# Kernel tuning notes

Measured on AMD Instinct MI355X. Metric: run time of the kernel, lower is better.

## Reference

```python
import jax, jax.numpy as jnp
import numpy as np

B, C_IN, H, W = 32, 3, 256, 256
PATCH = 16
E, C_OUT = 8, 8
C_PROJ = 16
NUM_CLASSES = 1000
SPP_LEVELS = (1, 2, 4)
GATE_STEEPNESS = 10.0


def _conv(x, w, b, pad):
    # x: [N,C,H,W], w: [O,C,kh,kw]
    y = jax.lax.conv_general_dilated(x, w, (1, 1), [(pad, pad), (pad, pad)],
                                     dimension_numbers=('NCHW', 'OIHW', 'NCHW'))
    return y + b[None, :, None, None]


def _forward(X, expert_w, expert_b, proj_w, proj_b, keys, threshold,
             final_w, final_b, lin_w, lin_b):
    Bx, C, Hx, Wx = X.shape
    h, w = Hx // PATCH, Wx // PATCH
    P = h * w
    # 1) patch extraction: [B,C,H,W] -> [B*P, C, ph, pw]
    xp = (X.reshape(Bx, C, h, PATCH, w, PATCH)
           .transpose(0, 2, 4, 1, 3, 5)
           .reshape(Bx * P, C, PATCH, PATCH))
    # 2) router: conv projection -> global avg pool -> key similarity -> softmax -> soft threshold gate
    proj = _conv(xp, proj_w, proj_b, 1)                 # [BP, 16, ph, pw]
    pooled = proj.mean(axis=(2, 3))                     # [BP, 16]
    scores = jax.nn.softmax(pooled @ keys.T, axis=-1)   # [BP, E]
    gate = scores * jax.nn.sigmoid((scores - threshold) * GATE_STEEPNESS)
    gate = gate / (gate.sum(axis=-1, keepdims=True) + 1e-9)
    gate = gate.reshape(Bx, P, E)
    # 3) all experts fused as one conv with E*C_OUT output channels (conv3x3 pad1 + ReLU)
    ew = expert_w.reshape(E * C_OUT, C, 3, 3)
    eb = expert_b.reshape(E * C_OUT)
    outs = jax.nn.relu(_conv(xp, ew, eb, 1))            # [BP, E*Cout, ph, pw]
    outs = outs.reshape(Bx, P, E, C_OUT, PATCH, PATCH)
    # 4) router-weighted combine over experts
    comb = jnp.einsum('bpe,bpeclm->bpclm', gate, outs)  # [B,P,Cout,ph,pw]
    # 5) reassemble patches -> [B, Cout, H, W]
    y = (comb.reshape(Bx, h, w, C_OUT, PATCH, PATCH)
             .transpose(0, 3, 1, 4, 2, 5)
             .reshape(Bx, C_OUT, h * PATCH, w * PATCH))
    # 6) final 1x1 conv with padding=4 (zero-pad input, bias added everywhere)
    ypad = jnp.pad(y, ((0, 0), (0, 0), (4, 4), (4, 4)))
    y = jnp.einsum('oc,bchw->bohw', final_w[:, :, 0, 0], ypad) + final_b[None, :, None, None]
    # 7) spatial pyramid pooling (levels 1,2,4) -> [B, Cout*21]
    Bc, Cc, Hc, Wc = y.shape
    feats = [y.reshape(Bc, Cc, l, Hc // l, l, Wc // l).mean(axis=(3, 5)).reshape(Bc, -1)
             for l in SPP_LEVELS]
    spp = jnp.concatenate(feats, axis=-1)
    # 8) classification head
    return spp @ lin_w + lin_b


def setup_inputs() -> dict:
    key = jax.random.key(0)
    ks = jax.random.split(key, 11)
    s = 0.1
    spp_dim = C_OUT * sum(l * l for l in SPP_LEVELS)  # 168
    return {
        'X': jax.random.normal(ks[0], (B, C_IN, H, W), jnp.float32),
        'expert_w': jax.random.normal(ks[1], (E, C_OUT, C_IN, 3, 3), jnp.float32) * s,
        'expert_b': jax.random.normal(ks[2], (E, C_OUT), jnp.float32) * s,
        'proj_w': jax.random.normal(ks[3], (C_PROJ, C_IN, 3, 3), jnp.float32) * s,
        'proj_b': jax.random.normal(ks[4], (C_PROJ,), jnp.float32) * s,
        'keys': jax.random.normal(ks[5], (E, C_PROJ), jnp.float32) * s,
        'threshold': jnp.array(0.125, jnp.float32),
        'final_w': jax.random.normal(ks[6], (C_OUT, C_OUT, 1, 1), jnp.float32) * s,
        'final_b': jax.random.normal(ks[7], (C_OUT,), jnp.float32) * s,
        'lin_w': jax.random.normal(ks[8], (spp_dim, NUM_CLASSES), jnp.float32) * s,
        'lin_b': jax.random.normal(ks[9], (NUM_CLASSES,), jnp.float32) * s,
    }


def reference(X, expert_w, expert_b, proj_w, proj_b, keys, threshold,
              final_w, final_b, lin_w, lin_b):
    return _forward(X, expert_w, expert_b, proj_w, proj_b, keys, threshold,
                    final_w, final_b, lin_w, lin_b)
```

## Files before the change

### kernel.cpp

```cpp
#include <hip/hip_runtime.h>
#include <hip/hip_bf16.h>
#include <math.h>


typedef short bf16x8 __attribute__((ext_vector_type(8)));
typedef float f32x4 __attribute__((ext_vector_type(4)));
typedef float pf2 __attribute__((ext_vector_type(2)));

__device__ __forceinline__ int cellOf(int r) {
    int rr = r + 4;
    return (rr >= 66) + (rr >= 132) + (rr >= 198);
}

__device__ __forceinline__ unsigned int packbf2(float lo, float hi) {
    __hip_bfloat162 h = __float22bfloat162_rn(make_float2(lo, hi));
    unsigned int u;
    __builtin_memcpy(&u, &h, 4);
    return u;
}

__global__ __launch_bounds__(256) void prep_kernel(
    const float* __restrict__ ew, const float* __restrict__ ebg,
    const float* __restrict__ pw, const float* __restrict__ pb,
    const float* __restrict__ keys, float* __restrict__ Sy,
    unsigned short* __restrict__ Bg, float* __restrict__ cbf)
{
    const int t = threadIdx.x;
    for (int i = t; i < 8192; i += 256) Sy[i] = 0.f;
    if (t < 72) {
        float sv[32];
        #pragma unroll
        for (int s = 0; s < 32; ++s) {
            int q, kx; bool zz = false;
            if (s < 16)       { q = s >> 1;  kx = s & 1; }
            else if (s < 18)  { q = 8;       kx = s - 16; }
            else if (s < 26)  { q = s - 18;  kx = 2; }
            else if (s == 26) { q = 8;       kx = 2; }
            else              { q = 0; kx = 0; zz = true; }
            const int ky = q / 3, c = q - ky * 3;
            const int widx = c * 9 + ky * 3 + kx;
            float a;
            if (t < 64) {
                a = ew[t * 27 + widx];
            } else {
                const int e = t - 64;
                a = 0.f;
                #pragma unroll
                for (int o = 0; o < 16; ++o)
                    a += keys[e * 16 + o] * pw[o * 27 + widx];
            }
            sv[s] = zz ? 0.f : a;
        }
        uint4 q0, q1, q2v, q3v;
        q0.x  = packbf2(sv[0],  sv[1]);  q0.y  = packbf2(sv[2],  sv[3]);
        q0.z  = packbf2(sv[4],  sv[5]);  q0.w  = packbf2(sv[6],  sv[7]);
        q1.x  = packbf2(sv[8],  sv[9]);  q1.y  = packbf2(sv[10], sv[11]);
        q1.z  = packbf2(sv[12], sv[13]); q1.w  = packbf2(sv[14], sv[15]);
        q2v.x = packbf2(sv[16], sv[17]); q2v.y = packbf2(sv[18], sv[19]);
        q2v.z = packbf2(sv[20], sv[21]); q2v.w = packbf2(sv[22], sv[23]);
        q3v.x = packbf2(sv[24], sv[25]); q3v.y = packbf2(sv[26], sv[27]);
        q3v.z = packbf2(sv[28], sv[29]); q3v.w = packbf2(sv[30], sv[31]);
        uint4* dst = reinterpret_cast<uint4*>(&Bg[t * 32]);
        dst[0] = q0; dst[1] = q1; dst[2] = q2v; dst[3] = q3v;
    }
    if (t >= 128 && t < 208) {
        const int i = t - 128;
        float c;
        if (i < 64) {
            c = ebg[i];
        } else {
            const int e = (i - 64) & 7;
            c = 0.f;
            #pragma unroll
            for (int o = 0; o < 16; ++o) c += keys[e * 16 + o] * pb[o];
        }
        cbf[i] = c;
    }
}

#define CONV_STEP(SB, ACCJ) do {                                            \
    uint4 pkv;                                                              \
    pkv.x = pkw[offp0 + (SB)];                                              \
    pkv.y = pkw[offp1 + (SB)];                                              \
    pkv.z = pkw[offp2 + (SB)];                                              \
    pkv.w = pkw[offp3 + (SB)];                                              \
    const bf16x8 afr = __builtin_bit_cast(bf16x8, pkv);                     \
    const f32x4 a0 = __builtin_amdgcn_mfma_f32_16x16x32_bf16(afr, bfr0, cbv0, 0, 0, 0); \
    const f32x4 a1 = __builtin_amdgcn_mfma_f32_16x16x32_bf16(afr, bfr1, cbv1, 0, 0, 0); \
    const f32x4 a2 = __builtin_amdgcn_mfma_f32_16x16x32_bf16(afr, bfr2, cbv2, 0, 0, 0); \
    const f32x4 a3 = __builtin_amdgcn_mfma_f32_16x16x32_bf16(afr, bfr3, cbv3, 0, 0, 0); \
    a4acc = __builtin_amdgcn_mfma_f32_16x16x32_bf16(afr, bfr4, a4acc, 0, 0, 0); \
    const pf2 z2_ = {0.f, 0.f};                                             \
    {                                                                       \
        const pf2 l_ = __builtin_elementwise_max((pf2)__builtin_shufflevector(a0, a0, 0, 1), z2_); \
        const pf2 h_ = __builtin_elementwise_max((pf2)__builtin_shufflevector(a0, a0, 2, 3), z2_); \
        pall2[0] += l_ + h_;                                                \
        if (ACCJ) psb2[0] += l_ * jm2lo + h_ * jm2hi;                       \
    }                                                                       \
    {                                                                       \
        const pf2 l_ = __builtin_elementwise_max((pf2)__builtin_shufflevector(a1, a1, 0, 1), z2_); \
        const pf2 h_ = __builtin_elementwise_max((pf2)__builtin_shufflevector(a1, a1, 2, 3), z2_); \
        pall2[1] += l_ + h_;                                                \
        if (ACCJ) psb2[1] += l_ * jm2lo + h_ * jm2hi;                       \
    }                                                                       \
    {                                                                       \
        const pf2 l_ = __builtin_elementwise_max((pf2)__builtin_shufflevector(a2, a2, 0, 1), z2_); \
        const pf2 h_ = __builtin_elementwise_max((pf2)__builtin_shufflevector(a2, a2, 2, 3), z2_); \
        pall2[2] += l_ + h_;                                                \
        if (ACCJ) psb2[2] += l_ * jm2lo + h_ * jm2hi;                       \
    }                                                                       \
    {                                                                       \
        const pf2 l_ = __builtin_elementwise_max((pf2)__builtin_shufflevector(a3, a3, 0, 1), z2_); \
        const pf2 h_ = __builtin_elementwise_max((pf2)__builtin_shufflevector(a3, a3, 2, 3), z2_); \
        pall2[3] += l_ + h_;                                                \
        if (ACCJ) psb2[3] += l_ * jm2lo + h_ * jm2hi;                       \
    }                                                                       \
} while (0)

#define GATES_FROM_RSUM()                                                   \
    rsum += __shfl_xor(rsum, 16);                                           \
    rsum += __shfl_xor(rsum, 32);                                           \
    float gv[4];                                                            \
    {                                                                       \
        float lg = rsum * (1.f / 256.f);                                    \
        float mx = fmaxf(lg, __shfl_xor(lg, 1));                            \
        mx = fmaxf(mx, __shfl_xor(mx, 2));                                  \
        mx = fmaxf(mx, __shfl_xor(mx, 4));                                  \
        float ex = __expf(lg - mx);                                         \
        float s = ex;                                                       \
        s += __shfl_xor(s, 1); s += __shfl_xor(s, 2); s += __shfl_xor(s, 4);\
        float sc = ex / s;                                                  \
        float g = sc / (1.f + __expf(-(sc - thr) * 10.f));                  \
        float gs = g;                                                       \
        gs += __shfl_xor(gs, 1); gs += __shfl_xor(gs, 2); gs += __shfl_xor(gs, 4); \
        float gn = g / (gs + 1e-9f);                                        \
        const int gb = (lid & 56);                                          \
        const int hb = (lid >> 3) & 1;                                      \
        gv[0] = __shfl(gn, gb | (0 + hb));                                  \
        gv[1] = __shfl(gn, gb | (2 + hb));                                  \
        gv[2] = __shfl(gn, gb | (4 + hb));                                  \
        gv[3] = __shfl(gn, gb | (6 + hb));                                  \
    }

__global__ __launch_bounds__(128, 4) void fused_kernel(
    const float* __restrict__ X, const unsigned short* __restrict__ Bg,
    const float* __restrict__ thr_p, const float* __restrict__ cbf,
    float* __restrict__ Sy)
{
    __shared__ __align__(16) unsigned int pk[2][1952];

    const int t = threadIdx.x;
    const int wid = t >> 6, lid = t & 63;
    const int r16 = lid & 15, kb = lid >> 4;

    const int wgid = blockIdx.x;
    const int virt = (wgid & 7) * 512 + (wgid >> 3);

    const int gp = (virt << 1) + wid;
    const int b = gp >> 8;
    const int pi = (gp >> 4) & 15, pj = gp & 15;
    const int rbase = pi << 4, cbase = pj << 4;

    unsigned int* pkw = pk[wid];
    const float thr = thr_p[0];

    const int lr = lid >> 2, lq = lid & 3;
    const float* xb = X + ((b * 3) << 16) + ((rbase + lr) << 8) + cbase + (lq << 2);
    const float4 xv0 = *reinterpret_cast<const float4*>(xb);
    const float4 xv1 = *reinterpret_cast<const float4*>(xb + 65536);
    const float4 xv2 = *reinterpret_cast<const float4*>(xb + 131072);

    const bf16x8 bfr0 = *reinterpret_cast<const bf16x8*>(&Bg[(r16) * 32 + (kb << 3)]);
    const bf16x8 bfr1 = *reinterpret_cast<const bf16x8*>(&Bg[(16 + r16) * 32 + (kb << 3)]);
    const bf16x8 bfr2 = *reinterpret_cast<const bf16x8*>(&Bg[(32 + r16) * 32 + (kb << 3)]);
    const bf16x8 bfr3 = *reinterpret_cast<const bf16x8*>(&Bg[(48 + r16) * 32 + (kb << 3)]);
    const bf16x8 bfr4 = *reinterpret_cast<const bf16x8*>(&Bg[(64 + (r16 & 7)) * 32 + (kb << 3)]);

    const float cbs0 = cbf[r16];
    const float cbs1 = cbf[16 + r16];
    const float cbs2 = cbf[32 + r16];
    const float cbs3 = cbf[48 + r16];
    const float cbs4 = cbf[64 + r16];

    if (lid < 54) {
        pkw[lid] = 0u;
        pkw[918 + lid] = 0u;
        pkw[976 + lid] = 0u;
        pkw[1894 + lid] = 0u;
    }
    if (lid < 48) {
        const int y3 = lid / 3;
        const int cp = lid - y3 * 3;
        pkw[976 + (y3 + 1) * 54 + cp * 18 + 16] = 0u;
    }
    __builtin_amdgcn_wave_barrier();

    float s0 = __shfl_up(xv0.w, 1);
    float s1 = __shfl_up(xv1.w, 1);
    float s2 = __shfl_up(xv2.w, 1);
    const float c0p = (lq == 0) ? 0.f : s0;
    const float c1p = (lq == 0) ? 0.f : s1;
    const float c2p = (lq == 0) ? 0.f : s2;
    float nxx = __shfl_down(xv0.x, 4);
    float nxy = __shfl_down(xv0.y, 4);
    float nxz = __shfl_down(xv0.z, 4);
    float nxw = __shfl_down(xv0.w, 4);
    if (lr == 15) { nxx = 0.f; nxy = 0.f; nxz = 0.f; nxw = 0.f; }

    {
        const int y = lr + 1;
        const int b2 = y * 54 + (lq << 2);
        unsigned int u0, u1, u2, u3;
        u0 = packbf2(c0p,   xv0.x); u1 = packbf2(xv0.x, xv0.y);
        u2 = packbf2(xv0.y, xv0.z); u3 = packbf2(xv0.z, xv0.w);
        *reinterpret_cast<uint2*>(&pkw[b2])      = make_uint2(u0, u1);
        *reinterpret_cast<uint2*>(&pkw[b2 + 2])  = make_uint2(u2, u3);
        u0 = packbf2(c1p,   xv1.x); u1 = packbf2(xv1.x, xv1.y);
        u2 = packbf2(xv1.y, xv1.z); u3 = packbf2(xv1.z, xv1.w);
        *reinterpret_cast<uint2*>(&pkw[b2 + 18]) = make_uint2(u0, u1);
        *reinterpret_cast<uint2*>(&pkw[b2 + 20]) = make_uint2(u2, u3);
        u0 = packbf2(c2p,   xv2.x); u1 = packbf2(xv2.x, xv2.y);
        u2 = packbf2(xv2.y, xv2.z); u3 = packbf2(xv2.z, xv2.w);
        *reinterpret_cast<uint2*>(&pkw[b2 + 36]) = make_uint2(u0, u1);
        *reinterpret_cast<uint2*>(&pkw[b2 + 38]) = make_uint2(u2, u3);

        const int bx = 976 + y * 54 + (lq << 2);
        u0 = packbf2(xv0.x, xv1.x); u1 = packbf2(xv0.y, xv1.y);
        u2 = packbf2(xv0.z, xv1.z); u3 = packbf2(xv0.w, xv1.w);
        *reinterpret_cast<uint2*>(&pkw[bx])      = make_uint2(u0, u1);
        *reinterpret_cast<uint2*>(&pkw[bx + 2])  = make_uint2(u2, u3);
        u0 = packbf2(xv1.x, xv2.x); u1 = packbf2(xv1.y, xv2.y);
        u2 = packbf2(xv1.z, xv2.z); u3 = packbf2(xv1.w, xv2.w);
        *reinterpret_cast<uint2*>(&pkw[bx + 18]) = make_uint2(u0, u1);
        *reinterpret_cast<uint2*>(&pkw[bx + 20]) = make_uint2(u2, u3);
        u0 = packbf2(xv2.x, nxx);  u1 = packbf2(xv2.y, nxy);
        u2 = packbf2(xv2.z, nxz);  u3 = packbf2(xv2.w, nxw);
        *reinterpret_cast<uint2*>(&pkw[bx + 36]) = make_uint2(u0, u1);
        *reinterpret_cast<uint2*>(&pkw[bx + 38]) = make_uint2(u2, u3);

        if (lr == 0) {
            const int b0 = 976 + 36 + (lq << 2);
            u0 = packbf2(0.f, xv0.x); u1 = packbf2(0.f, xv0.y);
            u2 = packbf2(0.f, xv0.z); u3 = packbf2(0.f, xv0.w);
            *reinterpret_cast<uint2*>(&pkw[b0])     = make_uint2(u0, u1);
            *reinterpret_cast<uint2*>(&pkw[b0 + 2]) = make_uint2(u2, u3);
        }
    }
    __builtin_amdgcn_wave_barrier();

    int offp0, offp1, offp2, offp3;
    if (kb < 2) {
        const int t0 = kb * 72 + r16;
        offp0 = t0; offp1 = t0 + 18; offp2 = t0 + 36; offp3 = t0 + 54;
    } else if (kb == 2) {
        offp0 = 144 + r16; offp1 = 977 + r16; offp2 = 1013 + r16; offp3 = 1049 + r16;
    } else {
        offp0 = 1085 + r16; offp1 = 1121 + r16; offp2 = 1121 + r16; offp3 = 1121 + r16;
    }

    const f32x4 cbv0 = {cbs0, cbs0, cbs0, cbs0};
    const f32x4 cbv1 = {cbs1, cbs1, cbs1, cbs1};
    const f32x4 cbv2 = {cbs2, cbs2, cbs2, cbs2};
    const f32x4 cbv3 = {cbs3, cbs3, cbs3, cbs3};
    const float rb16 = cbs4 * 16.f;
    f32x4 a4acc = {rb16, rb16, rb16, rb16};

    const int iA = cellOf(rbase), iB = cellOf(rbase + 15);
    const int jA = cellOf(cbase), jB = cellOf(cbase + 15);
    const int isp = (iA + 1) * 66 - 4 - rbase;
    const int jsp = (jA + 1) * 66 - 4 - cbase;
    const bool anySplit = (isp < 16) | (jsp < 16);

    const int bc16 = b << 4;
    const pf2 zz2 = {0.f, 0.f};

    if (!anySplit) {
        pf2 pall2[4] = {zz2, zz2, zz2, zz2};
        pf2 psb2[4]  = {zz2, zz2, zz2, zz2};
        pf2 jm2lo = zz2, jm2hi = zz2;
        #pragma unroll
        for (int mt = 0; mt < 16; ++mt) CONV_STEP(mt * 54, 0);

        float rsum = (a4acc[0] + a4acc[1]) + (a4acc[2] + a4acc[3]);
        GATES_FROM_RSUM();

        float tt = 0.f;
        #pragma unroll
        for (int nt = 0; nt < 4; ++nt)
            tt = fmaf(gv[nt], pall2[nt].x + pall2[nt].y, tt);
        tt += __shfl_xor(tt, 8);
        tt += __shfl_xor(tt, 16);
        tt += __shfl_xor(tt, 32);
        if (lid < 8)
            atomicAdd(&Sy[(iA * 4 + jA) * 512 + bc16 + lid], tt);
    } else {
        float jmask[4];
        #pragma unroll
        for (int r = 0; r < 4; ++r)
            jmask[r] = ((kb << 2) + r >= jsp) ? 1.f : 0.f;
        const pf2 jm2lo = {jmask[0], jmask[1]};
        const pf2 jm2hi = {jmask[2], jmask[3]};

        pf2 pall2[4] = {zz2, zz2, zz2, zz2};
        pf2 psb2[4]  = {zz2, zz2, zz2, zz2};
        const int m1 = isp < 16 ? isp : 16;

        int sb = 0;
        for (int mt = 0; mt < m1; ++mt) { CONV_STEP(sb, 1); sb += 54; }
        const float pa0_0 = pall2[0].x + pall2[0].y;
        const float pa0_1 = pall2[1].x + pall2[1].y;
        const float pa0_2 = pall2[2].x + pall2[2].y;
        const float pa0_3 = pall2[3].x + pall2[3].y;
        const float pb0_0 = psb2[0].x + psb2[0].y;
        const float pb0_1 = psb2[1].x + psb2[1].y;
        const float pb0_2 = psb2[2].x + psb2[2].y;
        const float pb0_3 = psb2[3].x + psb2[3].y;
        pall2[0] = pall2[1] = pall2[2] = pall2[3] = zz2;
        psb2[0] = psb2[1] = psb2[2] = psb2[3] = zz2;
        for (int mt = m1; mt < 16; ++mt) { CONV_STEP(sb, 1); sb += 54; }

        float rsum = (a4acc[0] + a4acc[1]) + (a4acc[2] + a4acc[3]);
        GATES_FROM_RSUM();

        float tTA = gv[0] * pa0_0 + gv[1] * pa0_1 + gv[2] * pa0_2 + gv[3] * pa0_3;
        float tTB = gv[0] * pb0_0 + gv[1] * pb0_1 + gv[2] * pb0_2 + gv[3] * pb0_3;
        float tBA = 0.f, tBB = 0.f;
        #pragma unroll
        for (int nt = 0; nt < 4; ++nt) {
            tBA = fmaf(gv[nt], pall2[nt].x + pall2[nt].y, tBA);
            tBB = fmaf(gv[nt], psb2[nt].x + psb2[nt].y, tBB);
        }
        #pragma unroll
        for (int m = 8; m <= 32; m <<= 1) {
            tTA += __shfl_xor(tTA, m);
            tTB += __shfl_xor(tTB, m);
            tBA += __shfl_xor(tBA, m);
            tBB += __shfl_xor(tBB, m);
        }
        if (lid < 8) {
            atomicAdd(&Sy[(iA * 4 + jA) * 512 + bc16 + lid], tTA - tTB);
            atomicAdd(&Sy[(iA * 4 + jB) * 512 + bc16 + lid], tTB);
            atomicAdd(&Sy[(iB * 4 + jA) * 512 + bc16 + lid], tBA - tBB);
            atomicAdd(&Sy[(iB * 4 + jB) * 512 + bc16 + lid], tBB);
        }
    }
}

__global__ __launch_bounds__(256) void head_kernel(
    const float* __restrict__ Sy, const float* __restrict__ fw,
    const float* __restrict__ fb, const float* __restrict__ lw,
    const float* __restrict__ lb, float* __restrict__ out)
{
    __shared__ float syl[128];
    __shared__ float s2[32];
    __shared__ float stot[8];
    __shared__ float spp[168];
    const int t = threadIdx.x;
    const int b = blockIdx.y;
    if (t < 128) syl[t] = Sy[(t & 15) * 512 + b * 16 + (t >> 4)];
    __syncthreads();
    if (t < 32) {
        int c = t >> 2, I = (t >> 1) & 1, J = t & 1;
        const float* p = &syl[c * 16];
        s2[t] = p[(2 * I) * 4 + 2 * J] + p[(2 * I) * 4 + 2 * J + 1] +
                p[(2 * I + 1) * 4 + 2 * J] + p[(2 * I + 1) * 4 + 2 * J + 1];
    } else if (t >= 32 && t < 40) {
        int c = t - 32;
        float s = 0.f;
        #pragma unroll
        for (int i2 = 0; i2 < 16; ++i2) s += syl[c * 16 + i2];
        stot[c] = s;
    }
    __syncthreads();
    if (t < 168) {
        float acc = 0.f;
        int o;
        if (t < 8) {
            o = t;
            #pragma unroll
            for (int c = 0; c < 8; ++c) acc += fw[o * 8 + c] * stot[c];
            acc *= (1.f / 69696.f);
        } else if (t < 40) {
            int m = t - 8; o = m >> 2; int q = m & 3;
            #pragma unroll
            for (int c = 0; c < 8; ++c) acc += fw[o * 8 + c] * s2[c * 4 + q];
            acc *= (1.f / 17424.f);
        } else {
            int m = t - 40; o = m >> 4; int cell = m & 15;
            #pragma unroll
            for (int c = 0; c < 8; ++c) acc += fw[o * 8 + c] * syl[c * 16 + cell];
            acc *= (1.f / 4356.f);
        }
        spp[t] = acc + fb[o];
    }
    __syncthreads();
    const int n = blockIdx.x * 256 + t;
    if (n < 1000) {
        float acc = lb[n];
        for (int k = 0; k < 168; ++k) acc = fmaf(spp[k], lw[k * 1000 + n], acc);
        out[b * 1000 + n] = acc;
    }
}

extern "C" void kernel_launch(void* const* d_in, const int* in_sizes, int n_in,
                              void* d_out, int out_size, void* d_ws, size_t ws_size,
                              hipStream_t stream) {
    const float* X    = (const float*)d_in[0];
    const float* ew   = (const float*)d_in[1];
    const float* eb   = (const float*)d_in[2];
    const float* pw   = (const float*)d_in[3];
    const float* pb   = (const float*)d_in[4];
    const float* keys = (const float*)d_in[5];
    const float* thr  = (const float*)d_in[6];
    const float* fw   = (const float*)d_in[7];
    const float* fb   = (const float*)d_in[8];
    const float* lw   = (const float*)d_in[9];
    const float* lb   = (const float*)d_in[10];
    float* out = (float*)d_out;
    float* Sy  = (float*)d_ws;
    unsigned short* Bg = (unsigned short*)((float*)d_ws + 8192);
    float* cbf = (float*)d_ws + 9344;

    prep_kernel<<<1, 256, 0, stream>>>(ew, eb, pw, pb, keys, Sy, Bg, cbf);
    fused_kernel<<<4096, 128, 0, stream>>>(X, Bg, thr, cbf, Sy);
    head_kernel<<<dim3(4, 32), 256, 0, stream>>>(Sy, fw, fb, lw, lb, out);
}
```

Measured before the change: 38.71 us.

## Spread atomic accumulators across slots, widen blocks to four waves, preload LDS fragments

The accumulator buffer grows fourfold so patches with different (pi,pj) parity write to separate slots, which cuts contention on the atomic adds; the head kernel sums the four slots when it reads them. The fused kernel moves from two to four waves per block, with half as many blocks and a larger LDS staging area. On the non-split path all A-fragments are read from LDS into registers before the MFMA loop, and zeroing uses float4 stores. The costs are more register pressure, which may lower occupancy, and a larger workspace.

```diff
diff --git a/kernel.cpp b/kernel.cpp
--- a/kernel.cpp
+++ b/kernel.cpp
@@ -26,7 +26,11 @@
     unsigned short* __restrict__ Bg, float* __restrict__ cbf)
 {
     const int t = threadIdx.x;
-    for (int i = t; i < 8192; i += 256) Sy[i] = 0.f;
+    {
+        float4* s4 = reinterpret_cast<float4*>(Sy);
+        const float4 z4 = make_float4(0.f, 0.f, 0.f, 0.f);
+        for (int i = t; i < 8192; i += 256) s4[i] = z4;
+    }
     if (t < 72) {
         float sv[32];
         #pragma unroll
@@ -78,13 +82,8 @@
     }
 }
 
-#define CONV_STEP(SB, ACCJ) do {                                            \
-    uint4 pkv;                                                              \
-    pkv.x = pkw[offp0 + (SB)];                                              \
-    pkv.y = pkw[offp1 + (SB)];                                              \
-    pkv.z = pkw[offp2 + (SB)];                                              \
-    pkv.w = pkw[offp3 + (SB)];                                              \
-    const bf16x8 afr = __builtin_bit_cast(bf16x8, pkv);                     \
+#define MFMA_CORE(PKV, ACCJ) do {                                           \
+    const bf16x8 afr = __builtin_bit_cast(bf16x8, (PKV));                   \
     const f32x4 a0 = __builtin_amdgcn_mfma_f32_16x16x32_bf16(afr, bfr0, cbv0, 0, 0, 0); \
     const f32x4 a1 = __builtin_amdgcn_mfma_f32_16x16x32_bf16(afr, bfr1, cbv1, 0, 0, 0); \
     const f32x4 a2 = __builtin_amdgcn_mfma_f32_16x16x32_bf16(afr, bfr2, cbv2, 0, 0, 0); \
@@ -117,6 +116,15 @@
     }                                                                       \
 } while (0)
 
+#define CONV_STEP_L(SB) do {                                                \
+    uint4 pkv;                                                              \
+    pkv.x = pkw[offp0 + (SB)];                                              \
+    pkv.y = pkw[offp1 + (SB)];                                              \
+    pkv.z = pkw[offp2 + (SB)];                                              \
+    pkv.w = pkw[offp3 + (SB)];                                              \
+    MFMA_CORE(pkv, 1);                                                      \
+} while (0)
+
 #define GATES_FROM_RSUM()                                                   \
     rsum += __shfl_xor(rsum, 16);                                           \
     rsum += __shfl_xor(rsum, 32);                                           \
@@ -142,21 +150,21 @@
         gv[3] = __shfl(gn, gb | (6 + hb));                                  \
     }
 
-__global__ __launch_bounds__(128, 4) void fused_kernel(
+__global__ __launch_bounds__(256, 3) void fused_kernel(
     const float* __restrict__ X, const unsigned short* __restrict__ Bg,
     const float* __restrict__ thr_p, const float* __restrict__ cbf,
     float* __restrict__ Sy)
 {
-    __shared__ __align__(16) unsigned int pk[2][1952];
+    __shared__ __align__(16) unsigned int pk[4][1952];
 
     const int t = threadIdx.x;
     const int wid = t >> 6, lid = t & 63;
     const int r16 = lid & 15, kb = lid >> 4;
 
     const int wgid = blockIdx.x;
-    const int virt = (wgid & 7) * 512 + (wgid >> 3);
-
-    const int gp = (virt << 1) + wid;
+    const int virt = (wgid & 7) * 256 + (wgid >> 3);
+
+    const int gp = (virt << 2) + wid;
     const int b = gp >> 8;
     const int pi = (gp >> 4) & 15, pj = gp & 15;
     const int rbase = pi << 4, cbase = pj << 4;
@@ -271,15 +279,30 @@
     const int jsp = (jA + 1) * 66 - 4 - cbase;
     const bool anySplit = (isp < 16) | (jsp < 16);
 
-    const int bc16 = b << 4;
+    const int slot = ((pi & 1) << 1) | (pj & 1);
+    const int lbase = (b << 6) + (slot << 4);
     const pf2 zz2 = {0.f, 0.f};
 
     if (!anySplit) {
+        unsigned int rg[16][4];
+        #pragma unroll
+        for (int mt = 0; mt < 16; ++mt) {
+            rg[mt][0] = pkw[offp0 + mt * 54];
+            rg[mt][1] = pkw[offp1 + mt * 54];
+            rg[mt][2] = pkw[offp2 + mt * 54];
+            rg[mt][3] = pkw[offp3 + mt * 54];
+        }
+
         pf2 pall2[4] = {zz2, zz2, zz2, zz2};
         pf2 psb2[4]  = {zz2, zz2, zz2, zz2};
         pf2 jm2lo = zz2, jm2hi = zz2;
         #pragma unroll
-        for (int mt = 0; mt < 16; ++mt) CONV_STEP(mt * 54, 0);
+        for (int mt = 0; mt < 16; ++mt) {
+            uint4 pkv;
+            pkv.x = rg[mt][0]; pkv.y = rg[mt][1];
+            pkv.z = rg[mt][2]; pkv.w = rg[mt][3];
+            MFMA_CORE(pkv, 0);
+        }
 
         float rsum = (a4acc[0] + a4acc[1]) + (a4acc[2] + a4acc[3]);
         GATES_FROM_RSUM();
@@ -292,7 +315,7 @@
         tt += __shfl_xor(tt, 16);
         tt += __shfl_xor(tt, 32);
         if (lid < 8)
-            atomicAdd(&Sy[(iA * 4 + jA) * 512 + bc16 + lid], tt);
+            atomicAdd(&Sy[(iA * 4 + jA) * 2048 + lbase + lid], tt);
     } else {
         float jmask[4];
         #pragma unroll
@@ -306,7 +329,7 @@
         const int m1 = isp < 16 ? isp : 16;
 
         int sb = 0;
-        for (int mt = 0; mt < m1; ++mt) { CONV_STEP(sb, 1); sb += 54; }
+        for (int mt = 0; mt < m1; ++mt) { CONV_STEP_L(sb); sb += 54; }
         const float pa0_0 = pall2[0].x + pall2[0].y;
         const float pa0_1 = pall2[1].x + pall2[1].y;
         const float pa0_2 = pall2[2].x + pall2[2].y;
@@ -317,7 +340,7 @@
         const float pb0_3 = psb2[3].x + psb2[3].y;
         pall2[0] = pall2[1] = pall2[2] = pall2[3] = zz2;
         psb2[0] = psb2[1] = psb2[2] = psb2[3] = zz2;
-        for (int mt = m1; mt < 16; ++mt) { CONV_STEP(sb, 1); sb += 54; }
+        for (int mt = m1; mt < 16; ++mt) { CONV_STEP_L(sb); sb += 54; }
 
         float rsum = (a4acc[0] + a4acc[1]) + (a4acc[2] + a4acc[3]);
         GATES_FROM_RSUM();
@@ -338,10 +361,10 @@
             tBB += __shfl_xor(tBB, m);
         }
         if (lid < 8) {
-            atomicAdd(&Sy[(iA * 4 + jA) * 512 + bc16 + lid], tTA - tTB);
-            atomicAdd(&Sy[(iA * 4 + jB) * 512 + bc16 + lid], tTB);
-            atomicAdd(&Sy[(iB * 4 + jA) * 512 + bc16 + lid], tBA - tBB);
-            atomicAdd(&Sy[(iB * 4 + jB) * 512 + bc16 + lid], tBB);
+            atomicAdd(&Sy[(iA * 4 + jA) * 2048 + lbase + lid], tTA - tTB);
+            atomicAdd(&Sy[(iA * 4 + jB) * 2048 + lbase + lid], tTB);
+            atomicAdd(&Sy[(iB * 4 + jA) * 2048 + lbase + lid], tBA - tBB);
+            atomicAdd(&Sy[(iB * 4 + jB) * 2048 + lbase + lid], tBB);
         }
     }
 }
@@ -357,7 +380,11 @@
     __shared__ float spp[168];
     const int t = threadIdx.x;
     const int b = blockIdx.y;
-    if (t < 128) syl[t] = Sy[(t & 15) * 512 + b * 16 + (t >> 4)];
+    if (t < 128) {
+        const int c = t >> 4, cell = t & 15;
+        const float* p = &Sy[cell * 2048 + (b << 6) + c];
+        syl[t] = (p[0] + p[16]) + (p[32] + p[48]);
+    }
     __syncthreads();
     if (t < 32) {
         int c = t >> 2, I = (t >> 1) & 1, J = t & 1;
@@ -418,10 +445,10 @@
     const float* lb   = (const float*)d_in[10];
     float* out = (float*)d_out;
     float* Sy  = (float*)d_ws;
-    unsigned short* Bg = (unsigned short*)((float*)d_ws + 8192);
-    float* cbf = (float*)d_ws + 9344;
+    unsigned short* Bg = (unsigned short*)((float*)d_ws + 32768);
+    float* cbf = (float*)d_ws + 33920;
 
     prep_kernel<<<1, 256, 0, stream>>>(ew, eb, pw, pb, keys, Sy, Bg, cbf);
-    fused_kernel<<<4096, 128, 0, stream>>>(X, Bg, thr, cbf, Sy);
+    fused_kernel<<<2048, 256, 0, stream>>>(X, Bg, thr, cbf, Sy);
     head_kernel<<<dim3(4, 32), 256, 0, stream>>>(Sy, fw, fb, lw, lb, out);
 }
```

After: 38.06 us. About the same (-1.7%).

## Fold prep into fused kernel and replace global atomics with per-patch partials

Applied to the files above, without the earlier changes.

Removes the single-block prep kernel launch by having each fused-kernel workgroup compute the bf16 expert/router weight fragments and biases into shared memory, with a block barrier before use. The fused kernel grows to 256 threads (four patches per block, 2048 blocks). Global atomicAdd accumulation into a zeroed Sy buffer is replaced by plain float4 stores of per-patch partial sums, which the head kernel now reduces with shared-memory atomics. This drops one launch, the zeroing pass and global atomic contention, at the cost of redundant weight prep in every block and extra reduction work in the head.

```diff
diff --git a/kernel.cpp b/kernel.cpp
--- a/kernel.cpp
+++ b/kernel.cpp
@@ -19,72 +19,8 @@
     return u;
 }
 
-__global__ __launch_bounds__(256) void prep_kernel(
-    const float* __restrict__ ew, const float* __restrict__ ebg,
-    const float* __restrict__ pw, const float* __restrict__ pb,
-    const float* __restrict__ keys, float* __restrict__ Sy,
-    unsigned short* __restrict__ Bg, float* __restrict__ cbf)
-{
-    const int t = threadIdx.x;
-    for (int i = t; i < 8192; i += 256) Sy[i] = 0.f;
-    if (t < 72) {
-        float sv[32];
-        #pragma unroll
-        for (int s = 0; s < 32; ++s) {
-            int q, kx; bool zz = false;
-            if (s < 16)       { q = s >> 1;  kx = s & 1; }
-            else if (s < 18)  { q = 8;       kx = s - 16; }
-            else if (s < 26)  { q = s - 18;  kx = 2; }
-            else if (s == 26) { q = 8;       kx = 2; }
-            else              { q = 0; kx = 0; zz = true; }
-            const int ky = q / 3, c = q - ky * 3;
-            const int widx = c * 9 + ky * 3 + kx;
-            float a;
-            if (t < 64) {
-                a = ew[t * 27 + widx];
-            } else {
-                const int e = t - 64;
-                a = 0.f;
-                #pragma unroll
-                for (int o = 0; o < 16; ++o)
-                    a += keys[e * 16 + o] * pw[o * 27 + widx];
-            }
-            sv[s] = zz ? 0.f : a;
-        }
-        uint4 q0, q1, q2v, q3v;
-        q0.x  = packbf2(sv[0],  sv[1]);  q0.y  = packbf2(sv[2],  sv[3]);
-        q0.z  = packbf2(sv[4],  sv[5]);  q0.w  = packbf2(sv[6],  sv[7]);
-        q1.x  = packbf2(sv[8],  sv[9]);  q1.y  = packbf2(sv[10], sv[11]);
-        q1.z  = packbf2(sv[12], sv[13]); q1.w  = packbf2(sv[14], sv[15]);
-        q2v.x = packbf2(sv[16], sv[17]); q2v.y = packbf2(sv[18], sv[19]);
-        q2v.z = packbf2(sv[20], sv[21]); q2v.w = packbf2(sv[22], sv[23]);
-        q3v.x = packbf2(sv[24], sv[25]); q3v.y = packbf2(sv[26], sv[27]);
-        q3v.z = packbf2(sv[28], sv[29]); q3v.w = packbf2(sv[30], sv[31]);
-        uint4* dst = reinterpret_cast<uint4*>(&Bg[t * 32]);
-        dst[0] = q0; dst[1] = q1; dst[2] = q2v; dst[3] = q3v;
-    }
-    if (t >= 128 && t < 208) {
-        const int i = t - 128;
-        float c;
-        if (i < 64) {
-            c = ebg[i];
-        } else {
-            const int e = (i - 64) & 7;
-            c = 0.f;
-            #pragma unroll
-            for (int o = 0; o < 16; ++o) c += keys[e * 16 + o] * pb[o];
-        }
-        cbf[i] = c;
-    }
-}
-
-#define CONV_STEP(SB, ACCJ) do {                                            \
-    uint4 pkv;                                                              \
-    pkv.x = pkw[offp0 + (SB)];                                              \
-    pkv.y = pkw[offp1 + (SB)];                                              \
-    pkv.z = pkw[offp2 + (SB)];                                              \
-    pkv.w = pkw[offp3 + (SB)];                                              \
-    const bf16x8 afr = __builtin_bit_cast(bf16x8, pkv);                     \
+#define MFMA_CORE(PKV, ACCJ) do {                                           \
+    const bf16x8 afr = __builtin_bit_cast(bf16x8, (PKV));                   \
     const f32x4 a0 = __builtin_amdgcn_mfma_f32_16x16x32_bf16(afr, bfr0, cbv0, 0, 0, 0); \
     const f32x4 a1 = __builtin_amdgcn_mfma_f32_16x16x32_bf16(afr, bfr1, cbv1, 0, 0, 0); \
     const f32x4 a2 = __builtin_amdgcn_mfma_f32_16x16x32_bf16(afr, bfr2, cbv2, 0, 0, 0); \
@@ -117,6 +53,15 @@
     }                                                                       \
 } while (0)
 
+#define CONV_STEP(SB, ACCJ) do {                                            \
+    uint4 pkv;                                                              \
+    pkv.x = pkw[offp0 + (SB)];                                              \
+    pkv.y = pkw[offp1 + (SB)];                                              \
+    pkv.z = pkw[offp2 + (SB)];                                              \
+    pkv.w = pkw[offp3 + (SB)];                                              \
+    MFMA_CORE(pkv, ACCJ);                                                   \
+} while (0)
+
 #define GATES_FROM_RSUM()                                                   \
     rsum += __shfl_xor(rsum, 16);                                           \
     rsum += __shfl_xor(rsum, 32);                                           \
@@ -142,21 +87,73 @@
         gv[3] = __shfl(gn, gb | (6 + hb));                                  \
     }
 
-__global__ __launch_bounds__(128, 4) void fused_kernel(
-    const float* __restrict__ X, const unsigned short* __restrict__ Bg,
-    const float* __restrict__ thr_p, const float* __restrict__ cbf,
-    float* __restrict__ Sy)
+__global__ __launch_bounds__(256, 4) void fused_kernel(
+    const float* __restrict__ X, const float* __restrict__ ew,
+    const float* __restrict__ ebg, const float* __restrict__ pw,
+    const float* __restrict__ pb, const float* __restrict__ keys,
+    const float* __restrict__ thr_p, float* __restrict__ Sout)
 {
-    __shared__ __align__(16) unsigned int pk[2][1952];
+    __shared__ __align__(16) unsigned int pk[4][1952];
+    __shared__ __align__(16) unsigned short Bgs[2304];
+    __shared__ float cbfs[80];
 
     const int t = threadIdx.x;
     const int wid = t >> 6, lid = t & 63;
     const int r16 = lid & 15, kb = lid >> 4;
 
+    if (t < 72) {
+        float sv[32];
+        #pragma unroll
+        for (int s = 0; s < 32; ++s) {
+            int q, kx; bool zz = false;
+            if (s < 16)       { q = s >> 1;  kx = s & 1; }
+            else if (s < 18)  { q = 8;       kx = s - 16; }
+            else if (s < 26)  { q = s - 18;  kx = 2; }
+            else if (s == 26) { q = 8;       kx = 2; }
+            else              { q = 0; kx = 0; zz = true; }
+            const int ky = q / 3, c = q - ky * 3;
+            const int widx = c * 9 + ky * 3 + kx;
+            float a;
+            if (t < 64) {
+                a = ew[t * 27 + widx];
+            } else {
+                const int e = t - 64;
+                a = 0.f;
+                #pragma unroll
+                for (int o = 0; o < 16; ++o)
+                    a += keys[e * 16 + o] * pw[o * 27 + widx];
+            }
+            sv[s] = zz ? 0.f : a;
+        }
+        uint4 q0, q1, q2v, q3v;
+        q0.x  = packbf2(sv[0],  sv[1]);  q0.y  = packbf2(sv[2],  sv[3]);
+        q0.z  = packbf2(sv[4],  sv[5]);  q0.w  = packbf2(sv[6],  sv[7]);
+        q1.x  = packbf2(sv[8],  sv[9]);  q1.y  = packbf2(sv[10], sv[11]);
+        q1.z  = packbf2(sv[12], sv[13]); q1.w  = packbf2(sv[14], sv[15]);
+        q2v.x = packbf2(sv[16], sv[17]); q2v.y = packbf2(sv[18], sv[19]);
+        q2v.z = packbf2(sv[20], sv[21]); q2v.w = packbf2(sv[22], sv[23]);
+        q3v.x = packbf2(sv[24], sv[25]); q3v.y = packbf2(sv[26], sv[27]);
+        q3v.z = packbf2(sv[28], sv[29]); q3v.w = packbf2(sv[30], sv[31]);
+        uint4* dst = reinterpret_cast<uint4*>(&Bgs[t * 32]);
+        dst[0] = q0; dst[1] = q1; dst[2] = q2v; dst[3] = q3v;
+    } else if (t >= 128 && t < 208) {
+        const int i = t - 128;
+        float c;
+        if (i < 64) {
+            c = ebg[i];
+        } else {
+            const int e = (i - 64) & 7;
+            c = 0.f;
+            #pragma unroll
+            for (int o = 0; o < 16; ++o) c += keys[e * 16 + o] * pb[o];
+        }
+        cbfs[i] = c;
+    }
+
     const int wgid = blockIdx.x;
-    const int virt = (wgid & 7) * 512 + (wgid >> 3);
-
-    const int gp = (virt << 1) + wid;
+    const int virt = (wgid & 7) * 256 + (wgid >> 3);
+
+    const int gp = (virt << 2) + wid;
     const int b = gp >> 8;
     const int pi = (gp >> 4) & 15, pj = gp & 15;
     const int rbase = pi << 4, cbase = pj << 4;
@@ -170,18 +167,6 @@
     const float4 xv1 = *reinterpret_cast<const float4*>(xb + 65536);
     const float4 xv2 = *reinterpret_cast<const float4*>(xb + 131072);
 
-    const bf16x8 bfr0 = *reinterpret_cast<const bf16x8*>(&Bg[(r16) * 32 + (kb << 3)]);
-    const bf16x8 bfr1 = *reinterpret_cast<const bf16x8*>(&Bg[(16 + r16) * 32 + (kb << 3)]);
-    const bf16x8 bfr2 = *reinterpret_cast<const bf16x8*>(&Bg[(32 + r16) * 32 + (kb << 3)]);
-    const bf16x8 bfr3 = *reinterpret_cast<const bf16x8*>(&Bg[(48 + r16) * 32 + (kb << 3)]);
-    const bf16x8 bfr4 = *reinterpret_cast<const bf16x8*>(&Bg[(64 + (r16 & 7)) * 32 + (kb << 3)]);
-
-    const float cbs0 = cbf[r16];
-    const float cbs1 = cbf[16 + r16];
-    const float cbs2 = cbf[32 + r16];
-    const float cbs3 = cbf[48 + r16];
-    const float cbs4 = cbf[64 + r16];
-
     if (lid < 54) {
         pkw[lid] = 0u;
         pkw[918 + lid] = 0u;
@@ -193,7 +178,20 @@
         const int cp = lid - y3 * 3;
         pkw[976 + (y3 + 1) * 54 + cp * 18 + 16] = 0u;
     }
-    __builtin_amdgcn_wave_barrier();
+
+    __syncthreads();
+
+    const bf16x8 bfr0 = *reinterpret_cast<const bf16x8*>(&Bgs[(r16) * 32 + (kb << 3)]);
+    const bf16x8 bfr1 = *reinterpret_cast<const bf16x8*>(&Bgs[(16 + r16) * 32 + (kb << 3)]);
+    const bf16x8 bfr2 = *reinterpret_cast<const bf16x8*>(&Bgs[(32 + r16) * 32 + (kb << 3)]);
+    const bf16x8 bfr3 = *reinterpret_cast<const bf16x8*>(&Bgs[(48 + r16) * 32 + (kb << 3)]);
+    const bf16x8 bfr4 = *reinterpret_cast<const bf16x8*>(&Bgs[(64 + (r16 & 7)) * 32 + (kb << 3)]);
+
+    const float cbs0 = cbfs[r16];
+    const float cbs1 = cbfs[16 + r16];
+    const float cbs2 = cbfs[32 + r16];
+    const float cbs3 = cbfs[48 + r16];
+    const float cbs4 = cbfs[64 + r16];
 
     float s0 = __shfl_up(xv0.w, 1);
     float s1 = __shfl_up(xv1.w, 1);
@@ -271,13 +269,13 @@
     const int jsp = (jA + 1) * 66 - 4 - cbase;
     const bool anySplit = (isp < 16) | (jsp < 16);
 
-    const int bc16 = b << 4;
     const pf2 zz2 = {0.f, 0.f};
 
     if (!anySplit) {
         pf2 pall2[4] = {zz2, zz2, zz2, zz2};
         pf2 psb2[4]  = {zz2, zz2, zz2, zz2};
         pf2 jm2lo = zz2, jm2hi = zz2;
+        (void)psb2; (void)jm2lo; (void)jm2hi;
         #pragma unroll
         for (int mt = 0; mt < 16; ++mt) CONV_STEP(mt * 54, 0);
 
@@ -291,8 +289,10 @@
         tt += __shfl_xor(tt, 8);
         tt += __shfl_xor(tt, 16);
         tt += __shfl_xor(tt, 32);
-        if (lid < 8)
-            atomicAdd(&Sy[(iA * 4 + jA) * 512 + bc16 + lid], tt);
+        if (lid < 8) {
+            float4 v = make_float4(tt, 0.f, 0.f, 0.f);
+            *reinterpret_cast<float4*>(&Sout[(gp << 5) + (lid << 2)]) = v;
+        }
     } else {
         float jmask[4];
         #pragma unroll
@@ -338,16 +338,14 @@
             tBB += __shfl_xor(tBB, m);
         }
         if (lid < 8) {
-            atomicAdd(&Sy[(iA * 4 + jA) * 512 + bc16 + lid], tTA - tTB);
-            atomicAdd(&Sy[(iA * 4 + jB) * 512 + bc16 + lid], tTB);
-            atomicAdd(&Sy[(iB * 4 + jA) * 512 + bc16 + lid], tBA - tBB);
-            atomicAdd(&Sy[(iB * 4 + jB) * 512 + bc16 + lid], tBB);
+            float4 v = make_float4(tTA, tTB, tBA, tBB);
+            *reinterpret_cast<float4*>(&Sout[(gp << 5) + (lid << 2)]) = v;
         }
     }
 }
 
 __global__ __launch_bounds__(256) void head_kernel(
-    const float* __restrict__ Sy, const float* __restrict__ fw,
+    const float* __restrict__ Sout, const float* __restrict__ fw,
     const float* __restrict__ fb, const float* __restrict__ lw,
     const float* __restrict__ lb, float* __restrict__ out)
 {
@@ -357,8 +355,30 @@
     __shared__ float spp[168];
     const int t = threadIdx.x;
     const int b = blockIdx.y;
-    if (t < 128) syl[t] = Sy[(t & 15) * 512 + b * 16 + (t >> 4)];
+
+    if (t < 128) syl[t] = 0.f;
     __syncthreads();
+
+    {
+        const int c = t & 7;
+        const int pg = t >> 3;
+        #pragma unroll
+        for (int k = 0; k < 8; ++k) {
+            const int p = pg * 8 + k;
+            const float4 v = *reinterpret_cast<const float4*>(
+                &Sout[((b << 8) + p) * 32 + (c << 2)]);
+            const int pi = p >> 4, pj = p & 15;
+            const int iA = cellOf(pi << 4), iB = cellOf((pi << 4) + 15);
+            const int jA = cellOf(pj << 4), jB = cellOf((pj << 4) + 15);
+            float* q = &syl[c << 4];
+            atomicAdd(&q[iA * 4 + jA], v.x - v.y);
+            atomicAdd(&q[iA * 4 + jB], v.y);
+            atomicAdd(&q[iB * 4 + jA], v.z - v.w);
+            atomicAdd(&q[iB * 4 + jB], v.w);
+        }
+    }
+    __syncthreads();
+
     if (t < 32) {
         int c = t >> 2, I = (t >> 1) & 1, J = t & 1;
         const float* p = &syl[c * 16];
@@ -416,12 +436,9 @@
     const float* fb   = (const float*)d_in[8];
     const float* lw   = (const float*)d_in[9];
     const float* lb   = (const float*)d_in[10];
-    float* out = (float*)d_out;
-    float* Sy  = (float*)d_ws;
-    unsigned short* Bg = (unsigned short*)((float*)d_ws + 8192);
-    float* cbf = (float*)d_ws + 9344;
-
-    prep_kernel<<<1, 256, 0, stream>>>(ew, eb, pw, pb, keys, Sy, Bg, cbf);
-    fused_kernel<<<4096, 128, 0, stream>>>(X, Bg, thr, cbf, Sy);
-    head_kernel<<<dim3(4, 32), 256, 0, stream>>>(Sy, fw, fb, lw, lb, out);
+    float* out  = (float*)d_out;
+    float* Sout = (float*)d_ws;
+
+    fused_kernel<<<2048, 256, 0, stream>>>(X, ew, eb, pw, pb, keys, thr, Sout);
+    head_kernel<<<dim3(4, 32), 256, 0, stream>>>(Sout, fw, fb, lw, lb, out);
 }
```

Measured after the change: 54.24 us. 1.4x slower.
